# Optimization experiments

Hardware: AMD Instinct MI355X
Metric: run time of the kernel (lower is better)

Reference implementation:

```python
import jax, jax.numpy as jnp
import numpy as np

POOL = 7          # pool_size (hard-coded 7x7 bin grid in source)
CROP = 2          # per-bin crop size: 14 // 7
ALPHA = 32        # channels per bin
H = W = 128
C = POOL * POOL * ALPHA  # 1568
NUM_ROIS = 4096


def setup_inputs() -> dict:
    key = jax.random.key(0)
    k_img, k_c, k_s = jax.random.split(key, 3)
    img = jax.random.normal(k_img, (1, H, W, C), dtype=jnp.float32)
    # valid normalized boxes [xmin, ymin, xmax, ymax] in [0, 1]
    cmin = jax.random.uniform(k_c, (1, NUM_ROIS, 2), dtype=jnp.float32) * 0.7
    size = 0.05 + jax.random.uniform(k_s, (1, NUM_ROIS, 2), dtype=jnp.float32) * 0.25
    rois = jnp.concatenate([cmin, cmin + size], axis=-1)  # (1, R, 4)
    return {"img": img, "rois": rois}


def _ps_roi_align(img, rois):
    # img: (1, H, W, 49*alpha) channels-last; rois: (1, R, 4) normalized xyxy
    h, w, c = img.shape[1], img.shape[2], img.shape[3]
    nbins = POOL * POOL
    alpha = c // nbins
    feat = img[0].reshape(h, w, nbins, alpha)  # channel group g <-> bin g

    xmin, ymin, xmax, ymax = (rois[0, :, i] for i in range(4))  # each (R,)
    step_y = (ymax - ymin) / POOL
    step_x = (xmax - xmin) / POOL

    g = jnp.arange(nbins)
    bx = (g // POOL).astype(img.dtype)  # bin order: bin_x outer, bin_y inner
    by = (g % POOL).astype(img.dtype)

    # per-roi per-bin sub-boxes, normalized coords, shape (R, B)
    y1 = ymin[:, None] + by[None, :] * step_y[:, None]
    x1 = xmin[:, None] + bx[None, :] * step_x[:, None]
    y2 = y1 + step_y[:, None]
    x2 = x1 + step_x[:, None]

    # tf.image.crop_and_resize sampling grid for crop size CROP (=2)
    t = jnp.arange(CROP, dtype=img.dtype) / (CROP - 1)  # (CROP,)
    ys = (y1[..., None] + (y2 - y1)[..., None] * t) * (h - 1)  # (R, B, CROP)
    xs = (x1[..., None] + (x2 - x1)[..., None] * t) * (w - 1)

    yg = ys[:, :, :, None]  # (R, B, CROP, 1)
    xg = xs[:, :, None, :]  # (R, B, 1, CROP)
    valid = (yg >= 0) & (yg <= h - 1) & (xg >= 0) & (xg <= w - 1)  # (R,B,CROP,CROP)

    y0f = jnp.floor(yg)
    x0f = jnp.floor(xg)
    wy = (yg - y0f)  # (R, B, CROP, 1)
    wx = (xg - x0f)  # (R, B, 1, CROP)

    y0 = jnp.clip(y0f.astype(jnp.int32), 0, h - 1)
    y1i = jnp.clip(y0 + 1, 0, h - 1)
    x0 = jnp.clip(x0f.astype(jnp.int32), 0, w - 1)
    x1i = jnp.clip(x0 + 1, 0, w - 1)

    bidx = g[None, :, None, None]  # (1, B, 1, 1) -> broadcasts with index grids

    def gather(yi, xi):
        yi, xi, bi = jnp.broadcast_arrays(yi, xi, bidx)
        return feat[yi, xi, bi]  # (R, B, CROP, CROP, alpha)

    val = (gather(y0, x0) * ((1 - wy) * (1 - wx))[..., None]
           + gather(y0, x1i) * ((1 - wy) * wx)[..., None]
           + gather(y1i, x0) * (wy * (1 - wx))[..., None]
           + gather(y1i, x1i) * (wy * wx)[..., None])
    val = jnp.where(valid[..., None], val, jnp.zeros((), img.dtype))

    pooled = val.max(axis=(2, 3))  # max over the CROPxCROP crop -> (R, B, alpha)
    return pooled.reshape(1, rois.shape[1], POOL, POOL, alpha)


def reference(img, rois):
    return _ps_roi_align(img, rois)
```

## Files before the change

### kernel.cpp

```cpp
#include <hip/hip_runtime.h>

#define POOLK 7
#define NBINS 49
#define ALPHA 32
#define C4N   8
#define HH    128
#define WW    128
#define NUM_ROIS 4096
#define F4_PER_PIX (NBINS * C4N)
#define NXCD 8
#define SLOTS_PER_XCD 784
#define CHUNKS_PER_PLANE 128

__global__ __launch_bounds__(256) void psroi_align_kernel(
    const float4* __restrict__ feat,
    const float4* __restrict__ rois4,
    float4* __restrict__ out4)
{
    const int bid   = blockIdx.x;
    const int xcd   = bid & (NXCD - 1);
    const int j     = bid >> 3;
    const int s     = xcd * SLOTS_PER_XCD + j;
    const int g     = s >> 7;
    const int chunk = s & (CHUNKS_PER_PLANE - 1);
    const int t     = (chunk << 8) + threadIdx.x;
    const int c4    = t & (C4N - 1);
    const int roi   = t >> 3;

    const float4 r = rois4[roi];

    const float step_x = (r.z - r.x) * (1.0f / POOLK);
    const float step_y = (r.w - r.y) * (1.0f / POOLK);

    const int p = g / POOLK;
    const int q = g % POOLK;

    const float x1 = r.x + (float)p * step_x;
    const float y1 = r.y + (float)q * step_y;

    const float scale = (float)(HH - 1);
    float ys[2], xs[2];
    ys[0] = y1 * scale;
    ys[1] = (y1 + step_y) * scale;
    xs[0] = x1 * scale;
    xs[1] = (x1 + step_x) * scale;

    float wy[2], wx[2];
    bool  vy[2], vx[2];
    int   yrow[4], xcol[4];
    #pragma unroll
    for (int sa = 0; sa < 2; ++sa) {
        const float yg = ys[sa];
        vy[sa] = (yg >= 0.0f) && (yg <= (float)(HH - 1));
        const float y0f = floorf(yg);
        wy[sa] = yg - y0f;
        int y0 = min(max((int)y0f, 0), HH - 1);
        yrow[2 * sa]     = y0;
        yrow[2 * sa + 1] = min(y0 + 1, HH - 1);

        const float xg = xs[sa];
        vx[sa] = (xg >= 0.0f) && (xg <= (float)(WW - 1));
        const float x0f = floorf(xg);
        wx[sa] = xg - x0f;
        int x0 = min(max((int)x0f, 0), WW - 1);
        xcol[2 * sa]     = x0;
        xcol[2 * sa + 1] = min(x0 + 1, WW - 1);
    }

    const int gbase = g * C4N + c4;

    int rowoff[4], coloff[4];
    #pragma unroll
    for (int i = 0; i < 4; ++i) {
        rowoff[i] = yrow[i] * (WW * F4_PER_PIX) + gbase;
        coloff[i] = xcol[i] * F4_PER_PIX;
    }

    float4 ld[16];
    #pragma unroll
    for (int rr = 0; rr < 4; ++rr) {
        #pragma unroll
        for (int cc = 0; cc < 4; ++cc) {
            ld[rr * 4 + cc] = feat[rowoff[rr] + coloff[cc]];
        }
    }

    float4 vmax;
    vmax.x = -INFINITY; vmax.y = -INFINITY; vmax.z = -INFINITY; vmax.w = -INFINITY;

    #pragma unroll
    for (int sy = 0; sy < 2; ++sy) {
        #pragma unroll
        for (int sx = 0; sx < 2; ++sx) {
            const float w11 = wy[sy] * wx[sx];
            const float w10 = wy[sy] - w11;
            const float w01 = wx[sx] - w11;
            const float w00 = 1.0f - wy[sy] - wx[sx] + w11;

            const float4 v00 = ld[(2 * sy)     * 4 + (2 * sx)];
            const float4 v01 = ld[(2 * sy)     * 4 + (2 * sx + 1)];
            const float4 v10 = ld[(2 * sy + 1) * 4 + (2 * sx)];
            const float4 v11 = ld[(2 * sy + 1) * 4 + (2 * sx + 1)];

            float4 v;
            v.x = v00.x * w00 + v01.x * w01 + v10.x * w10 + v11.x * w11;
            v.y = v00.y * w00 + v01.y * w01 + v10.y * w10 + v11.y * w11;
            v.z = v00.z * w00 + v01.z * w01 + v10.z * w10 + v11.z * w11;
            v.w = v00.w * w00 + v01.w * w01 + v10.w * w10 + v11.w * w11;

            if (!(vy[sy] && vx[sx])) { v.x = 0.0f; v.y = 0.0f; v.z = 0.0f; v.w = 0.0f; }

            vmax.x = fmaxf(vmax.x, v.x);
            vmax.y = fmaxf(vmax.y, v.y);
            vmax.z = fmaxf(vmax.z, v.z);
            vmax.w = fmaxf(vmax.w, v.w);
        }
    }

    out4[(roi * NBINS + g) * C4N + c4] = vmax;
}

extern "C" void kernel_launch(void* const* d_in, const int* in_sizes, int n_in,
                              void* d_out, int out_size, void* d_ws, size_t ws_size,
                              hipStream_t stream) {
    const float4* feat = (const float4*)d_in[0];
    const float4* rois = (const float4*)d_in[1];
    float4* out = (float4*)d_out;

    const int grid = NXCD * SLOTS_PER_XCD;
    psroi_align_kernel<<<grid, 256, 0, stream>>>(feat, rois, out);
}
```

Before: 165.0 us.

## Sort ROIs by Morton-coded center to improve gather cache locality

Adds a single-block pre-pass that buckets ROIs by a 4-bit-per-axis Morton code of their box centers and writes a permutation into the workspace. The main kernel then processes ROIs in that spatially sorted order, so neighbouring threads gather from nearby feature pixels and can share L2/MALL lines. The float4 code also moves to ext_vector_type arithmetic. The cost is an extra kernel launch, a serial prefix scan in one thread, and an indirect lookup per thread.

```diff
diff --git a/kernel.cpp b/kernel.cpp
--- a/kernel.cpp
+++ b/kernel.cpp
@@ -1,4 +1,6 @@
 #include <hip/hip_runtime.h>
+
+typedef float f32x4 __attribute__((ext_vector_type(4)));
 
 #define POOLK 7
 #define NBINS 49
@@ -12,10 +14,58 @@
 #define SLOTS_PER_XCD 784
 #define CHUNKS_PER_PLANE 128
 
+__global__ __launch_bounds__(256) void roi_sort_kernel(
+    const f32x4* __restrict__ rois4,
+    int* __restrict__ perm)
+{
+    __shared__ int hist[256];
+    __shared__ int base[256];
+    const int t = threadIdx.x;
+
+    hist[t] = 0;
+    __syncthreads();
+
+    int key[16];
+    #pragma unroll
+    for (int i = 0; i < 16; ++i) {
+        const int roi = i * 256 + t;
+        const f32x4 r = rois4[roi];
+        const float cx = 0.5f * (r[0] + r[2]);
+        const float cy = 0.5f * (r[1] + r[3]);
+        int kx = (int)(cx * 16.0f);
+        int ky = (int)(cy * 16.0f);
+        kx = min(15, max(0, kx));
+        ky = min(15, max(0, ky));
+        int k = 0;
+        #pragma unroll
+        for (int b = 0; b < 4; ++b) {
+            k |= ((kx >> b) & 1) << (2 * b + 1);
+            k |= ((ky >> b) & 1) << (2 * b);
+        }
+        key[i] = k;
+        atomicAdd(&hist[k], 1);
+    }
+    __syncthreads();
+
+    if (t == 0) {
+        int acc = 0;
+        for (int k = 0; k < 256; ++k) { base[k] = acc; acc += hist[k]; }
+    }
+    __syncthreads();
+
+    #pragma unroll
+    for (int i = 0; i < 16; ++i) {
+        const int roi = i * 256 + t;
+        const int pos = atomicAdd(&base[key[i]], 1);
+        perm[pos] = roi;
+    }
+}
+
 __global__ __launch_bounds__(256) void psroi_align_kernel(
-    const float4* __restrict__ feat,
-    const float4* __restrict__ rois4,
-    float4* __restrict__ out4)
+    const f32x4* __restrict__ feat,
+    const f32x4* __restrict__ rois4,
+    const int* __restrict__ perm,
+    f32x4* __restrict__ out4)
 {
     const int bid   = blockIdx.x;
     const int xcd   = bid & (NXCD - 1);
@@ -23,20 +73,21 @@
     const int s     = xcd * SLOTS_PER_XCD + j;
     const int g     = s >> 7;
     const int chunk = s & (CHUNKS_PER_PLANE - 1);
-    const int t     = (chunk << 8) + threadIdx.x;
-    const int c4    = t & (C4N - 1);
-    const int roi   = t >> 3;
+    const int tpl   = (chunk << 8) + threadIdx.x;
+    const int c4    = tpl & (C4N - 1);
+    const int slot  = tpl >> 3;
+    const int roi   = perm[slot];
 
-    const float4 r = rois4[roi];
+    const f32x4 r = rois4[roi];
 
-    const float step_x = (r.z - r.x) * (1.0f / POOLK);
-    const float step_y = (r.w - r.y) * (1.0f / POOLK);
+    const float step_x = (r[2] - r[0]) * (1.0f / POOLK);
+    const float step_y = (r[3] - r[1]) * (1.0f / POOLK);
 
     const int p = g / POOLK;
     const int q = g % POOLK;
 
-    const float x1 = r.x + (float)p * step_x;
-    const float y1 = r.y + (float)q * step_y;
+    const float x1 = r[0] + (float)p * step_x;
+    const float y1 = r[1] + (float)q * step_y;
 
     const float scale = (float)(HH - 1);
     float ys[2], xs[2];
@@ -76,7 +127,7 @@
         coloff[i] = xcol[i] * F4_PER_PIX;
     }
 
-    float4 ld[16];
+    f32x4 ld[16];
     #pragma unroll
     for (int rr = 0; rr < 4; ++rr) {
         #pragma unroll
@@ -85,8 +136,7 @@
         }
     }
 
-    float4 vmax;
-    vmax.x = -INFINITY; vmax.y = -INFINITY; vmax.z = -INFINITY; vmax.w = -INFINITY;
+    f32x4 vmax = { -INFINITY, -INFINITY, -INFINITY, -INFINITY };
 
     #pragma unroll
     for (int sy = 0; sy < 2; ++sy) {
@@ -97,23 +147,17 @@
             const float w01 = wx[sx] - w11;
             const float w00 = 1.0f - wy[sy] - wx[sx] + w11;
 
-            const float4 v00 = ld[(2 * sy)     * 4 + (2 * sx)];
-            const float4 v01 = ld[(2 * sy)     * 4 + (2 * sx + 1)];
-            const float4 v10 = ld[(2 * sy + 1) * 4 + (2 * sx)];
-            const float4 v11 = ld[(2 * sy + 1) * 4 + (2 * sx + 1)];
+            const f32x4 v00 = ld[(2 * sy)     * 4 + (2 * sx)];
+            const f32x4 v01 = ld[(2 * sy)     * 4 + (2 * sx + 1)];
+            const f32x4 v10 = ld[(2 * sy + 1) * 4 + (2 * sx)];
+            const f32x4 v11 = ld[(2 * sy + 1) * 4 + (2 * sx + 1)];
 
-            float4 v;
-            v.x = v00.x * w00 + v01.x * w01 + v10.x * w10 + v11.x * w11;
-            v.y = v00.y * w00 + v01.y * w01 + v10.y * w10 + v11.y * w11;
-            v.z = v00.z * w00 + v01.z * w01 + v10.z * w10 + v11.z * w11;
-            v.w = v00.w * w00 + v01.w * w01 + v10.w * w10 + v11.w * w11;
+            f32x4 v = v00 * w00 + v01 * w01 + v10 * w10 + v11 * w11;
 
-            if (!(vy[sy] && vx[sx])) { v.x = 0.0f; v.y = 0.0f; v.z = 0.0f; v.w = 0.0f; }
+            if (!(vy[sy] && vx[sx])) v = (f32x4){0.0f, 0.0f, 0.0f, 0.0f};
 
-            vmax.x = fmaxf(vmax.x, v.x);
-            vmax.y = fmaxf(vmax.y, v.y);
-            vmax.z = fmaxf(vmax.z, v.z);
-            vmax.w = fmaxf(vmax.w, v.w);
+            #pragma unroll
+            for (int jj = 0; jj < 4; ++jj) vmax[jj] = fmaxf(vmax[jj], v[jj]);
         }
     }
 
@@ -123,10 +167,13 @@
 extern "C" void kernel_launch(void* const* d_in, const int* in_sizes, int n_in,
                               void* d_out, int out_size, void* d_ws, size_t ws_size,
                               hipStream_t stream) {
-    const float4* feat = (const float4*)d_in[0];
-    const float4* rois = (const float4*)d_in[1];
-    float4* out = (float4*)d_out;
+    const f32x4* feat = (const f32x4*)d_in[0];
+    const f32x4* rois = (const f32x4*)d_in[1];
+    f32x4* out = (f32x4*)d_out;
+    int* perm = (int*)d_ws;
+
+    roi_sort_kernel<<<1, 256, 0, stream>>>(rois, perm);
 
     const int grid = NXCD * SLOTS_PER_XCD;
-    psroi_align_kernel<<<grid, 256, 0, stream>>>(feat, rois, out);
+    psroi_align_kernel<<<grid, 256, 0, stream>>>(feat, rois, perm, out);
 }
```

Result: slower. 174.9 us (+6.0%).
